# Performance work log

Hardware: AMD Instinct MI355X
Metric: run time of the kernel (lower is better)

## Reference

```python
import jax, jax.numpy as jnp
import numpy as np

N = 8192          # num_points
RADIUS = 0.5


def _make_curve(num_points):
    # Reproduces the interp1d-based turbo-coil curve from __init__ (linear interp).
    xk = np.array([-2, -1, 0, 1, 1, 0, -1, -1, 0, 1, 2], dtype=np.float64)
    zk = np.array([0, 0, 1, 0, -1, 0, 1, 0, -1, 0, 0], dtype=np.float64)
    yk = np.array([0, 0, 1, 1, -1, -1, -1, 1, 1, 0, 0], dtype=np.float64)
    t = np.linspace(0.0, 1.0, len(xk))
    s = np.linspace(0.0, 1.0, num_points)
    return (np.interp(s, t, xk).astype(np.float32),
            np.interp(s, t, yk).astype(np.float32),
            np.interp(s, t, zk).astype(np.float32))


def setup_inputs() -> dict:
    x, y, z = _make_curve(N)
    return {"x": jnp.asarray(x), "y": jnp.asarray(y), "z": jnp.asarray(z)}


def _cdist(a, b):
    # pairwise Euclidean distance, safe at zero (subgradient 0 like torch.cdist)
    d2 = jnp.sum(a * a, -1, keepdims=True) - 2.0 * (a @ b.T) + jnp.sum(b * b, -1)
    d2 = jnp.maximum(d2, 0.0)
    safe = jnp.where(d2 > 0.0, d2, 1.0)
    return jnp.where(d2 > 0.0, jnp.sqrt(safe), 0.0)


def _mask_distances(dist, min_dist):
    # Original: for each row i, scan j = i, i+1, ... and overwrite entries with
    # min_dist+1 while dist[i,j] <= min_dist, breaking at the first entry that
    # exceeds min_dist (the j in range(i,0) loop is empty, so only the forward
    # scan matters). Vectorized: contiguous prefix-run starting at the diagonal.
    n = dist.shape[0]
    rows = jnp.arange(n)[:, None]
    cols = jnp.arange(n)[None, :]
    upper = cols >= rows
    cond = dist <= min_dist
    # cumprod along each row, seeded with 1 (True) left of the diagonal, so that
    # run[i,j] = all(cond[i, i..j]) for j >= i
    run = jnp.cumprod(jnp.where(upper, cond, True).astype(jnp.int32), axis=1)
    mask = upper & (run > 0)
    return jnp.where(mask, min_dist + 1.0, dist)


def _puffer_loss(p2d, low, high):
    # PufferZone(points_2d, -1.0, 1.0, x): out-of-bounds penalty on [low, high]
    return jax.nn.relu(p2d - high) + jax.nn.relu(low - p2d)


def _noise_loss(p2d):
    # noise_reduction_loss: penalize curvature (squared second differences)
    d2 = p2d[2:] - 2.0 * p2d[1:-1] + p2d[:-2]
    return d2 * d2


def reference(x, y, z, scale=1.0):
    p2d = jnp.stack([y, z], axis=1)          # [N, 2]
    p3d = jnp.stack([x, y, z], axis=1)       # [N, 3]

    fixed = _puffer_loss(p2d, -1.0, 1.0)

    dist = _cdist(p3d, p3d)                  # [N, N]
    min_dist = RADIUS * 2.0 * scale
    dist_mask = _mask_distances(dist, min_dist)
    intersect = jax.nn.relu(min_dist - dist_mask)

    noise = _noise_loss(p2d)

    # dist_loss (WeightedEuclideanDistance) taken as the pairwise cdist sum
    return (jnp.sum(fixed)
            + jnp.sum(dist) / 10000.0
            + jnp.sum(intersect)
            + jnp.sum(noise) * 10.0)
```

## Files before the change

kernel.cpp:

```cpp
#include <hip/hip_runtime.h>

constexpr int N = 8192;
constexpr float TRI = 33558528.0f;

__device__ __forceinline__ float fsqrt(float v) { return __builtin_amdgcn_sqrtf(v); }


__global__ __launch_bounds__(256)
void pack_kernel(const float* __restrict__ x, const float* __restrict__ y,
                 const float* __restrict__ z, float4* __restrict__ p4) {
    const int i = blockIdx.x * 256 + threadIdx.x;
    p4[i] = make_float4(x[i], y[i], z[i], 0.f);
}

__global__ __launch_bounds__(256, 8)
void main_kernel(const float4* __restrict__ p4,
                 float* __restrict__ row_sd, float* __restrict__ row_sm,
                 float* __restrict__ row_corr) {
    const int tid  = threadIdx.x;
    const int lane = tid & 63;
    const int wave = tid >> 6;

    if (blockIdx.x < 1024) {
        const int b       = blockIdx.x;
        const int topBase = 4 * b;
        const int botBase = N - 4 * (b + 1);

        float xr[8], yr[8], zr[8];
#pragma unroll
        for (int r = 0; r < 4; ++r) {
            const float4 pt = p4[topBase + r];
            const float4 pb = p4[botBase + r];
            xr[r]     = pt.x; yr[r]     = pt.y; zr[r]     = pt.z;
            xr[4 + r] = pb.x; yr[4 + r] = pb.y; zr[4 + r] = pb.z;
        }
        float sd[8], sm[8];
#pragma unroll
        for (int r = 0; r < 8; ++r) { sd[r] = 0.f; sm[r] = 0.f; }

#pragma unroll
        for (int g = 0; g < 2; ++g) {
            const int base = g ? botBase : topBase;
            const int ro   = g * 4;

            {
                const int    j  = base + tid;
                const int    jc = (j < N) ? j : (N - 1);
                const float4 p  = p4[jc];
#pragma unroll
                for (int r = 0; r < 4; ++r) {
                    const float dx = p.x - xr[ro + r], dy = p.y - yr[ro + r], dz = p.z - zr[ro + r];
                    const float d  = fsqrt(dx * dx + dy * dy + dz * dz);
                    if (j < N && tid >= r) { sd[ro + r] += d; sm[ro + r] += fminf(d, 1.f); }
                }
            }
            int j0 = base + 256;
            if (j0 + 256 <= N) {
                float4 p = p4[j0 + tid];
                while (true) {
                    const float4 c    = p;
                    const bool   more = (j0 + 512 <= N);
                    if (more) p = p4[j0 + 256 + tid];
#pragma unroll
                    for (int r = 0; r < 4; ++r) {
                        const float dx = c.x - xr[ro + r], dy = c.y - yr[ro + r], dz = c.z - zr[ro + r];
                        const float d  = fsqrt(dx * dx + dy * dy + dz * dz);
                        sd[ro + r] += d; sm[ro + r] += fminf(d, 1.f);
                    }
                    j0 += 256;
                    if (!more) break;
                }
            }
            if (j0 < N) {
                const int j = j0 + tid;
                if (j < N) {
                    const float4 p = p4[j];
#pragma unroll
                    for (int r = 0; r < 4; ++r) {
                        const float dx = p.x - xr[ro + r], dy = p.y - yr[ro + r], dz = p.z - zr[ro + r];
                        const float d  = fsqrt(dx * dx + dy * dy + dz * dz);
                        sd[ro + r] += d; sm[ro + r] += fminf(d, 1.f);
                    }
                }
            }
        }

        __shared__ float lsd[4][8];
        __shared__ float lsm[4][8];
#pragma unroll
        for (int r = 0; r < 8; ++r) {
            float a = sd[r], c = sm[r];
#pragma unroll
            for (int off = 32; off; off >>= 1) {
                a += __shfl_down(a, off);
                c += __shfl_down(c, off);
            }
            if (lane == 0) { lsd[wave][r] = a; lsm[wave][r] = c; }
        }
        __syncthreads();
        if (tid < 8) {
            const float a = lsd[0][tid] + lsd[1][tid] + lsd[2][tid] + lsd[3][tid];
            const float c = lsm[0][tid] + lsm[1][tid] + lsm[2][tid] + lsm[3][tid];
            const int   i = (tid < 4) ? (topBase + tid) : (botBase + tid - 4);
            row_sd[i] = a;
            row_sm[i] = c;
        }
    } else {
        const int cb = blockIdx.x - 1024;
#pragma unroll
        for (int rr = 0; rr < 2; ++rr) {
            const int    i  = 8 * cb + 2 * wave + rr;
            const float4 pi = p4[i];
            float corr = 0.f;
            int   jb   = i;
            float4 a  = p4[min(jb + lane,      N - 1)];
            float4 bq = p4[min(jb + 64 + lane, N - 1)];
            while (true) {
                const float4 na = p4[min(jb + 128 + lane, N - 1)];
                const float4 nb = p4[min(jb + 192 + lane, N - 1)];
                const int j0i = jb + lane, j1i = jb + 64 + lane;
                float dx = a.x - pi.x, dy = a.y - pi.y, dz = a.z - pi.z;
                const float d0 = fsqrt(dx * dx + dy * dy + dz * dz);
                dx = bq.x - pi.x; dy = bq.y - pi.y; dz = bq.z - pi.z;
                const float d1 = fsqrt(dx * dx + dy * dy + dz * dz);
                const unsigned long long m0 = __ballot(j0i >= N || d0 > 1.f);
                const unsigned long long m1 = __ballot(j1i >= N || d1 > 1.f);
                int stop;
                if (m0)      stop = __builtin_ctzll(m0);
                else if (m1) stop = 64 + __builtin_ctzll(m1);
                else         stop = 128;
                if (lane < stop)      corr += 1.f - d0;
                if (64 + lane < stop) corr += 1.f - d1;
                if (stop < 128) break;
                jb += 128;
                a = na; bq = nb;
            }
#pragma unroll
            for (int off = 32; off; off >>= 1) corr += __shfl_down(corr, off);
            if (lane == 0) row_corr[i] = corr;
        }
    }
}

__global__ __launch_bounds__(256)
void partial_kernel(const float* __restrict__ y, const float* __restrict__ z,
                    const float* __restrict__ row_sd, const float* __restrict__ row_sm,
                    const float* __restrict__ row_corr, float* __restrict__ partials) {
    const int tid = threadIdx.x;
    const int i   = blockIdx.x * 256 + tid;
    float v[5];
    v[0] = row_sd[i];
    v[1] = row_sm[i];
    v[2] = row_corr[i];
    const float yv = y[i], zv = z[i];
    v[3] = fmaxf(yv - 1.f, 0.f) + fmaxf(-1.f - yv, 0.f)
         + fmaxf(zv - 1.f, 0.f) + fmaxf(-1.f - zv, 0.f);
    v[4] = 0.f;
    if (i < N - 2) {
        const float d2y = y[i + 2] - 2.f * y[i + 1] + y[i];
        const float d2z = z[i + 2] - 2.f * z[i + 1] + z[i];
        v[4] = d2y * d2y + d2z * d2z;
    }
    const int lane = tid & 63, wave = tid >> 6;
    __shared__ float s[4][5];
#pragma unroll
    for (int c = 0; c < 5; ++c) {
        float a = v[c];
#pragma unroll
        for (int off = 32; off; off >>= 1) a += __shfl_down(a, off);
        if (lane == 0) s[wave][c] = a;
    }
    __syncthreads();
    if (tid == 0) {
#pragma unroll
        for (int c = 0; c < 5; ++c)
            partials[blockIdx.x * 5 + c] = s[0][c] + s[1][c] + s[2][c] + s[3][c];
    }
}

__global__ __launch_bounds__(64)
void final_kernel(const float* __restrict__ partials, float* __restrict__ out) {
    const int tid = threadIdx.x;
    float a[5] = {0.f, 0.f, 0.f, 0.f, 0.f};
    if (tid < 32) {
#pragma unroll
        for (int c = 0; c < 5; ++c) a[c] = partials[tid * 5 + c];
    }
#pragma unroll
    for (int c = 0; c < 5; ++c) {
#pragma unroll
        for (int off = 16; off; off >>= 1) a[c] += __shfl_down(a[c], off, 32);
    }
    if (tid == 0) {
        const float A = a[0], M = a[1], C = a[2], fix = a[3], noise = a[4];
        out[0] = fix + (2.f * A) / 10000.f
               + (2.f * (TRI - M) - (float)N - C) + 10.f * noise;
    }
}

extern "C" void kernel_launch(void* const* d_in, const int* in_sizes, int n_in,
                              void* d_out, int out_size, void* d_ws, size_t ws_size,
                              hipStream_t stream) {
    const float* x = (const float*)d_in[0];
    const float* y = (const float*)d_in[1];
    const float* z = (const float*)d_in[2];
    float* out      = (float*)d_out;
    float4* p4      = (float4*)d_ws;
    float* row_sd   = (float*)(p4 + N);
    float* row_sm   = row_sd + N;
    float* row_corr = row_sm + N;
    float* partials = row_corr + N;

    pack_kernel<<<N / 256, 256, 0, stream>>>(x, y, z, p4);
    main_kernel<<<2048, 256, 0, stream>>>(p4, row_sd, row_sm, row_corr);
    partial_kernel<<<32, 256, 0, stream>>>(y, z, row_sd, row_sm, row_corr, partials);
    final_kernel<<<1, 64, 0, stream>>>(partials, out);
}
```

Baseline: 29.26 us.

## Widen correction scan to 512-point double-buffered chunks and merge final reductions

Result: slower. 41.31 us (median of 2 runs) (+41.2%).

```diff
diff --git a/kernel.cpp b/kernel.cpp
--- a/kernel.cpp
+++ b/kernel.cpp
@@ -13,7 +13,7 @@
     p4[i] = make_float4(x[i], y[i], z[i], 0.f);
 }
 
-__global__ __launch_bounds__(256, 8)
+__global__ __launch_bounds__(256, 4)
 void main_kernel(const float4* __restrict__ p4,
                  float* __restrict__ row_sd, float* __restrict__ row_sm,
                  float* __restrict__ row_corr) {
@@ -108,32 +108,62 @@
     } else {
         const int cb = blockIdx.x - 1024;
 #pragma unroll
-        for (int rr = 0; rr < 2; ++rr) {
-            const int    i  = 8 * cb + 2 * wave + rr;
+        for (int rr = 0; rr < 4; ++rr) {
+            const int    i  = 16 * cb + 4 * wave + rr;
             const float4 pi = p4[i];
             float corr = 0.f;
             int   jb   = i;
-            float4 a  = p4[min(jb + lane,      N - 1)];
-            float4 bq = p4[min(jb + 64 + lane, N - 1)];
+
+            float4 A[8], B[8];
+#pragma unroll
+            for (int q = 0; q < 8; ++q)
+                A[q] = p4[min(jb + q * 64 + lane, N - 1)];
+
             while (true) {
-                const float4 na = p4[min(jb + 128 + lane, N - 1)];
-                const float4 nb = p4[min(jb + 192 + lane, N - 1)];
-                const int j0i = jb + lane, j1i = jb + 64 + lane;
-                float dx = a.x - pi.x, dy = a.y - pi.y, dz = a.z - pi.z;
-                const float d0 = fsqrt(dx * dx + dy * dy + dz * dz);
-                dx = bq.x - pi.x; dy = bq.y - pi.y; dz = bq.z - pi.z;
-                const float d1 = fsqrt(dx * dx + dy * dy + dz * dz);
-                const unsigned long long m0 = __ballot(j0i >= N || d0 > 1.f);
-                const unsigned long long m1 = __ballot(j1i >= N || d1 > 1.f);
-                int stop;
-                if (m0)      stop = __builtin_ctzll(m0);
-                else if (m1) stop = 64 + __builtin_ctzll(m1);
-                else         stop = 128;
-                if (lane < stop)      corr += 1.f - d0;
-                if (64 + lane < stop) corr += 1.f - d1;
-                if (stop < 128) break;
-                jb += 128;
-                a = na; bq = nb;
+#pragma unroll
+                for (int q = 0; q < 8; ++q)
+                    B[q] = p4[min(jb + 512 + q * 64 + lane, N - 1)];
+                {
+                    float d[8];
+                    unsigned long long bm[8];
+#pragma unroll
+                    for (int q = 0; q < 8; ++q) {
+                        const float dx = A[q].x - pi.x, dy = A[q].y - pi.y, dz = A[q].z - pi.z;
+                        d[q] = fsqrt(dx * dx + dy * dy + dz * dz);
+                        bm[q] = __ballot((jb + q * 64 + lane >= N) || (d[q] > 1.f));
+                    }
+                    int stop = 512;
+#pragma unroll
+                    for (int q = 0; q < 8; ++q)
+                        if (stop == 512 && bm[q]) stop = q * 64 + __builtin_ctzll(bm[q]);
+#pragma unroll
+                    for (int q = 0; q < 8; ++q)
+                        if (q * 64 + lane < stop) corr += 1.f - d[q];
+                    if (stop < 512) break;
+                    jb += 512;
+                }
+#pragma unroll
+                for (int q = 0; q < 8; ++q)
+                    A[q] = p4[min(jb + 512 + q * 64 + lane, N - 1)];
+                {
+                    float d[8];
+                    unsigned long long bm[8];
+#pragma unroll
+                    for (int q = 0; q < 8; ++q) {
+                        const float dx = B[q].x - pi.x, dy = B[q].y - pi.y, dz = B[q].z - pi.z;
+                        d[q] = fsqrt(dx * dx + dy * dy + dz * dz);
+                        bm[q] = __ballot((jb + q * 64 + lane >= N) || (d[q] > 1.f));
+                    }
+                    int stop = 512;
+#pragma unroll
+                    for (int q = 0; q < 8; ++q)
+                        if (stop == 512 && bm[q]) stop = q * 64 + __builtin_ctzll(bm[q]);
+#pragma unroll
+                    for (int q = 0; q < 8; ++q)
+                        if (q * 64 + lane < stop) corr += 1.f - d[q];
+                    if (stop < 512) break;
+                    jb += 512;
+                }
             }
 #pragma unroll
             for (int off = 32; off; off >>= 1) corr += __shfl_down(corr, off);
@@ -143,58 +173,40 @@
 }
 
 __global__ __launch_bounds__(256)
-void partial_kernel(const float* __restrict__ y, const float* __restrict__ z,
-                    const float* __restrict__ row_sd, const float* __restrict__ row_sm,
-                    const float* __restrict__ row_corr, float* __restrict__ partials) {
+void reduce_kernel(const float* __restrict__ y, const float* __restrict__ z,
+                   const float* __restrict__ row_sd, const float* __restrict__ row_sm,
+                   const float* __restrict__ row_corr, float* __restrict__ out) {
     const int tid = threadIdx.x;
-    const int i   = blockIdx.x * 256 + tid;
-    float v[5];
-    v[0] = row_sd[i];
-    v[1] = row_sm[i];
-    v[2] = row_corr[i];
-    const float yv = y[i], zv = z[i];
-    v[3] = fmaxf(yv - 1.f, 0.f) + fmaxf(-1.f - yv, 0.f)
-         + fmaxf(zv - 1.f, 0.f) + fmaxf(-1.f - zv, 0.f);
-    v[4] = 0.f;
-    if (i < N - 2) {
-        const float d2y = y[i + 2] - 2.f * y[i + 1] + y[i];
-        const float d2z = z[i + 2] - 2.f * z[i + 1] + z[i];
-        v[4] = d2y * d2y + d2z * d2z;
-    }
+    float A = 0.f, M = 0.f, C = 0.f, fix = 0.f, noise = 0.f;
+    for (int i = tid; i < N; i += 256) {
+        A += row_sd[i];
+        M += row_sm[i];
+        C += row_corr[i];
+        const float yv = y[i], zv = z[i];
+        fix += fmaxf(yv - 1.f, 0.f) + fmaxf(-1.f - yv, 0.f)
+             + fmaxf(zv - 1.f, 0.f) + fmaxf(-1.f - zv, 0.f);
+        if (i < N - 2) {
+            const float d2y = y[i + 2] - 2.f * y[i + 1] + y[i];
+            const float d2z = z[i + 2] - 2.f * z[i + 1] + z[i];
+            noise += d2y * d2y + d2z * d2z;
+        }
+    }
+    __shared__ float s[5][4];
     const int lane = tid & 63, wave = tid >> 6;
-    __shared__ float s[4][5];
+    float v[5] = {A, M, C, fix, noise};
 #pragma unroll
     for (int c = 0; c < 5; ++c) {
-        float a = v[c];
-#pragma unroll
-        for (int off = 32; off; off >>= 1) a += __shfl_down(a, off);
-        if (lane == 0) s[wave][c] = a;
+#pragma unroll
+        for (int off = 32; off; off >>= 1) v[c] += __shfl_down(v[c], off);
+        if (lane == 0) s[c][wave] = v[c];
     }
     __syncthreads();
     if (tid == 0) {
-#pragma unroll
-        for (int c = 0; c < 5; ++c)
-            partials[blockIdx.x * 5 + c] = s[0][c] + s[1][c] + s[2][c] + s[3][c];
-    }
-}
-
-__global__ __launch_bounds__(64)
-void final_kernel(const float* __restrict__ partials, float* __restrict__ out) {
-    const int tid = threadIdx.x;
-    float a[5] = {0.f, 0.f, 0.f, 0.f, 0.f};
-    if (tid < 32) {
-#pragma unroll
-        for (int c = 0; c < 5; ++c) a[c] = partials[tid * 5 + c];
-    }
-#pragma unroll
-    for (int c = 0; c < 5; ++c) {
-#pragma unroll
-        for (int off = 16; off; off >>= 1) a[c] += __shfl_down(a[c], off, 32);
-    }
-    if (tid == 0) {
-        const float A = a[0], M = a[1], C = a[2], fix = a[3], noise = a[4];
-        out[0] = fix + (2.f * A) / 10000.f
-               + (2.f * (TRI - M) - (float)N - C) + 10.f * noise;
+        float t[5];
+#pragma unroll
+        for (int c = 0; c < 5; ++c) t[c] = s[c][0] + s[c][1] + s[c][2] + s[c][3];
+        out[0] = t[3] + (2.f * t[0]) / 10000.f
+               + (2.f * (TRI - t[1]) - (float)N - t[2]) + 10.f * t[4];
     }
 }
 
@@ -209,10 +221,8 @@
     float* row_sd   = (float*)(p4 + N);
     float* row_sm   = row_sd + N;
     float* row_corr = row_sm + N;
-    float* partials = row_corr + N;
 
     pack_kernel<<<N / 256, 256, 0, stream>>>(x, y, z, p4);
-    main_kernel<<<2048, 256, 0, stream>>>(p4, row_sd, row_sm, row_corr);
-    partial_kernel<<<32, 256, 0, stream>>>(y, z, row_sd, row_sm, row_corr, partials);
-    final_kernel<<<1, 64, 0, stream>>>(partials, out);
-}
+    main_kernel<<<1536, 256, 0, stream>>>(p4, row_sd, row_sm, row_corr);
+    reduce_kernel<<<1, 256, 0, stream>>>(y, z, row_sd, row_sm, row_corr, out);
+}
```

## Merge partial and final reductions into one kernel; hoist row coords to SGPRs

Applied to the files above, without the earlier changes.

Result: slower. 39.99 us (+36.7%).

```diff
diff --git a/kernel.cpp b/kernel.cpp
--- a/kernel.cpp
+++ b/kernel.cpp
@@ -4,6 +4,9 @@
 constexpr float TRI = 33558528.0f;
 
 __device__ __forceinline__ float fsqrt(float v) { return __builtin_amdgcn_sqrtf(v); }
+__device__ __forceinline__ float sgpr(float v) {
+    return __int_as_float(__builtin_amdgcn_readfirstlane(__float_as_int(v)));
+}
 
 
 __global__ __launch_bounds__(256)
@@ -31,8 +34,8 @@
         for (int r = 0; r < 4; ++r) {
             const float4 pt = p4[topBase + r];
             const float4 pb = p4[botBase + r];
-            xr[r]     = pt.x; yr[r]     = pt.y; zr[r]     = pt.z;
-            xr[4 + r] = pb.x; yr[4 + r] = pb.y; zr[4 + r] = pb.z;
+            xr[r]     = sgpr(pt.x); yr[r]     = sgpr(pt.y); zr[r]     = sgpr(pt.z);
+            xr[4 + r] = sgpr(pb.x); yr[4 + r] = sgpr(pb.y); zr[4 + r] = sgpr(pb.z);
         }
         float sd[8], sm[8];
 #pragma unroll
@@ -42,6 +45,15 @@
         for (int g = 0; g < 2; ++g) {
             const int base = g ? botBase : topBase;
             const int ro   = g * 4;
+
+            auto body = [&](const float4& c) {
+#pragma unroll
+                for (int r = 0; r < 4; ++r) {
+                    const float dx = c.x - xr[ro + r], dy = c.y - yr[ro + r], dz = c.z - zr[ro + r];
+                    const float d  = fsqrt(dx * dx + dy * dy + dz * dz);
+                    sd[ro + r] += d; sm[ro + r] += fminf(d, 1.f);
+                }
+            };
 
             {
                 const int    j  = base + tid;
@@ -54,23 +66,28 @@
                     if (j < N && tid >= r) { sd[ro + r] += d; sm[ro + r] += fminf(d, 1.f); }
                 }
             }
-            int j0 = base + 256;
-            if (j0 + 256 <= N) {
-                float4 p = p4[j0 + tid];
-                while (true) {
-                    const float4 c    = p;
-                    const bool   more = (j0 + 512 <= N);
-                    if (more) p = p4[j0 + 256 + tid];
-#pragma unroll
-                    for (int r = 0; r < 4; ++r) {
-                        const float dx = c.x - xr[ro + r], dy = c.y - yr[ro + r], dz = c.z - zr[ro + r];
-                        const float d  = fsqrt(dx * dx + dy * dy + dz * dz);
-                        sd[ro + r] += d; sm[ro + r] += fminf(d, 1.f);
-                    }
-                    j0 += 256;
-                    if (!more) break;
-                }
-            }
+
+            const int first = base + 256;
+            const int nfull = (N - first) / 256;
+            float4 pA, pB;
+            if (nfull >= 1) pA = p4[first + tid];
+            if (nfull >= 2) pB = p4[first + 256 + tid];
+            int t = 0;
+            for (; t + 2 <= nfull; t += 2) {
+                {
+                    const float4 c = pA;
+                    if (t + 2 < nfull) pA = p4[first + (t + 2) * 256 + tid];
+                    body(c);
+                }
+                {
+                    const float4 c = pB;
+                    if (t + 3 < nfull) pB = p4[first + (t + 3) * 256 + tid];
+                    body(c);
+                }
+            }
+            if (t < nfull) body(pA);
+
+            const int j0 = first + nfull * 256;
             if (j0 < N) {
                 const int j = j0 + tid;
                 if (j < N) {
@@ -143,58 +160,40 @@
 }
 
 __global__ __launch_bounds__(256)
-void partial_kernel(const float* __restrict__ y, const float* __restrict__ z,
-                    const float* __restrict__ row_sd, const float* __restrict__ row_sm,
-                    const float* __restrict__ row_corr, float* __restrict__ partials) {
+void reduce_kernel(const float* __restrict__ y, const float* __restrict__ z,
+                   const float* __restrict__ row_sd, const float* __restrict__ row_sm,
+                   const float* __restrict__ row_corr, float* __restrict__ out) {
     const int tid = threadIdx.x;
-    const int i   = blockIdx.x * 256 + tid;
-    float v[5];
-    v[0] = row_sd[i];
-    v[1] = row_sm[i];
-    v[2] = row_corr[i];
-    const float yv = y[i], zv = z[i];
-    v[3] = fmaxf(yv - 1.f, 0.f) + fmaxf(-1.f - yv, 0.f)
-         + fmaxf(zv - 1.f, 0.f) + fmaxf(-1.f - zv, 0.f);
-    v[4] = 0.f;
-    if (i < N - 2) {
-        const float d2y = y[i + 2] - 2.f * y[i + 1] + y[i];
-        const float d2z = z[i + 2] - 2.f * z[i + 1] + z[i];
-        v[4] = d2y * d2y + d2z * d2z;
-    }
+    float A = 0.f, M = 0.f, C = 0.f, fix = 0.f, noise = 0.f;
+    for (int i = tid; i < N; i += 256) {
+        A += row_sd[i];
+        M += row_sm[i];
+        C += row_corr[i];
+        const float yv = y[i], zv = z[i];
+        fix += fmaxf(yv - 1.f, 0.f) + fmaxf(-1.f - yv, 0.f)
+             + fmaxf(zv - 1.f, 0.f) + fmaxf(-1.f - zv, 0.f);
+        if (i < N - 2) {
+            const float d2y = y[i + 2] - 2.f * y[i + 1] + y[i];
+            const float d2z = z[i + 2] - 2.f * z[i + 1] + z[i];
+            noise += d2y * d2y + d2z * d2z;
+        }
+    }
+    __shared__ float s[5][4];
     const int lane = tid & 63, wave = tid >> 6;
-    __shared__ float s[4][5];
+    float v[5] = {A, M, C, fix, noise};
 #pragma unroll
     for (int c = 0; c < 5; ++c) {
-        float a = v[c];
-#pragma unroll
-        for (int off = 32; off; off >>= 1) a += __shfl_down(a, off);
-        if (lane == 0) s[wave][c] = a;
+#pragma unroll
+        for (int off = 32; off; off >>= 1) v[c] += __shfl_down(v[c], off);
+        if (lane == 0) s[c][wave] = v[c];
     }
     __syncthreads();
     if (tid == 0) {
-#pragma unroll
-        for (int c = 0; c < 5; ++c)
-            partials[blockIdx.x * 5 + c] = s[0][c] + s[1][c] + s[2][c] + s[3][c];
-    }
-}
-
-__global__ __launch_bounds__(64)
-void final_kernel(const float* __restrict__ partials, float* __restrict__ out) {
-    const int tid = threadIdx.x;
-    float a[5] = {0.f, 0.f, 0.f, 0.f, 0.f};
-    if (tid < 32) {
-#pragma unroll
-        for (int c = 0; c < 5; ++c) a[c] = partials[tid * 5 + c];
-    }
-#pragma unroll
-    for (int c = 0; c < 5; ++c) {
-#pragma unroll
-        for (int off = 16; off; off >>= 1) a[c] += __shfl_down(a[c], off, 32);
-    }
-    if (tid == 0) {
-        const float A = a[0], M = a[1], C = a[2], fix = a[3], noise = a[4];
-        out[0] = fix + (2.f * A) / 10000.f
-               + (2.f * (TRI - M) - (float)N - C) + 10.f * noise;
+        float t[5];
+#pragma unroll
+        for (int c = 0; c < 5; ++c) t[c] = s[c][0] + s[c][1] + s[c][2] + s[c][3];
+        out[0] = t[3] + (2.f * t[0]) / 10000.f
+               + (2.f * (TRI - t[1]) - (float)N - t[2]) + 10.f * t[4];
     }
 }
 
@@ -209,10 +208,8 @@
     float* row_sd   = (float*)(p4 + N);
     float* row_sm   = row_sd + N;
     float* row_corr = row_sm + N;
-    float* partials = row_corr + N;
 
     pack_kernel<<<N / 256, 256, 0, stream>>>(x, y, z, p4);
     main_kernel<<<2048, 256, 0, stream>>>(p4, row_sd, row_sm, row_corr);
-    partial_kernel<<<32, 256, 0, stream>>>(y, z, row_sd, row_sm, row_corr, partials);
-    final_kernel<<<1, 64, 0, stream>>>(partials, out);
-}
+    reduce_kernel<<<1, 256, 0, stream>>>(y, z, row_sd, row_sm, row_corr, out);
+}
```
